# Performance work log

Measured on AMD Instinct MI355X. Metric: run time of the kernel, lower is better.

The kernel has to match this reference:

```python
import jax, jax.numpy as jnp
from jax import lax
import numpy as np

KPAD = 2  # padding for 5x5 kernel, 'same' output

def setup_inputs() -> dict:
    key = jax.random.key(0)
    x = jax.random.normal(key, (16, 8, 512, 512), dtype=jnp.float32)
    # fixed 5x5 averaging kernel, matching torch.ones(5,5)/25
    weight = jnp.ones((1, 1, 5, 5), dtype=jnp.float32) / 25.0
    return {"x": x, "weight": weight}

def reference(x, weight):
    # Per-channel (depthwise) 5x5 box blur. The torch code loops conv2d over
    # split channels; a single grouped conv with feature_group_count=C is the
    # same math in one fused op.
    C = x.shape[1]
    k = jnp.tile(weight, (C, 1, 1, 1))  # (C,1,5,5) OIHW with groups=C
    return lax.conv_general_dilated(
        x, k,
        window_strides=(1, 1),
        padding=[(KPAD, KPAD), (KPAD, KPAD)],
        dimension_numbers=("NCHW", "OIHW", "NCHW"),
        feature_group_count=C,
    )
```

## Files before the change

### kernel.cpp

```cpp
#include <hip/hip_runtime.h>


#define H 512
#define W 512
#define TH 16
#define LROWS (TH + 4)
#define LSTRIDE (W + 8)

__global__ __launch_bounds__(256) void avefilter_kernel(
    const float* __restrict__ x, const float* __restrict__ wgt,
    float* __restrict__ out) {
    __shared__ float smem[LROWS * LSTRIDE];

    const int tid   = threadIdx.x;
    const int r0    = blockIdx.x * TH;
    const int plane = blockIdx.y;

    const float* in   = x   + (size_t)plane * (H * W);
    float*       outp = out + (size_t)plane * (H * W);
    const float scale = wgt[0];

    for (int i = tid; i < LROWS * 8; i += 256) {
        int lr = i >> 3;
        int c  = i & 7;
        int lc = (c < 4) ? c : (W + c);
        smem[lr * LSTRIDE + lc] = 0.0f;
    }

    for (int i = tid; i < LROWS * (W / 4); i += 256) {
        int lr = i >> 7;
        int vc = i & 127;
        int gr = r0 - 2 + lr;
        float4 v = make_float4(0.f, 0.f, 0.f, 0.f);
        if (gr >= 0 && gr < H) {
            v = ((const float4*)(in + (size_t)gr * W))[vc];
        }
        ((float4*)(smem + lr * LSTRIDE + 4))[vc] = v;
    }
    __syncthreads();

    #pragma unroll
    for (int ci = 0; ci < 2; ++ci) {
        const int xcol = tid + ci * 256;
        const float* bcol = smem + xcol + 2;

        float h[5];
        #pragma unroll
        for (int i = 0; i < 5; ++i) {
            const float* b = bcol + i * LSTRIDE;
            h[i] = b[0] + b[1] + b[2] + b[3] + b[4];
        }

        #pragma unroll
        for (int r = 0; r < TH; ++r) {
            float s = h[0] + h[1] + h[2] + h[3] + h[4];
            outp[(size_t)(r0 + r) * W + xcol] = s * scale;
            if (r < TH - 1) {
                const float* b = bcol + (r + 5) * LSTRIDE;
                h[r % 5] = b[0] + b[1] + b[2] + b[3] + b[4];
            }
        }
    }
}

extern "C" void kernel_launch(void* const* d_in, const int* in_sizes, int n_in,
                              void* d_out, int out_size, void* d_ws, size_t ws_size,
                              hipStream_t stream) {
    const float* x   = (const float*)d_in[0];
    const float* wgt = (const float*)d_in[1];
    float* out = (float*)d_out;

    dim3 grid(H / TH, 16 * 8);
    dim3 block(256);
    avefilter_kernel<<<grid, block, 0, stream>>>(x, wgt, out);
}
```

Before: 240.8 us.

## Replace shared-memory tiling with per-wave register strips and lane shuffles

```diff
diff --git a/kernel.cpp b/kernel.cpp
--- a/kernel.cpp
+++ b/kernel.cpp
@@ -3,63 +3,67 @@
 
 #define H 512
 #define W 512
-#define TH 16
-#define LROWS (TH + 4)
-#define LSTRIDE (W + 8)
+#define RSTRIP 16
 
-__global__ __launch_bounds__(256) void avefilter_kernel(
+__global__ __launch_bounds__(256, 4) void avefilter_kernel(
     const float* __restrict__ x, const float* __restrict__ wgt,
-    float* __restrict__ out) {
-    __shared__ float smem[LROWS * LSTRIDE];
-
-    const int tid   = threadIdx.x;
-    const int r0    = blockIdx.x * TH;
-    const int plane = blockIdx.y;
+    float* __restrict__ out)
+{
+    const int lane  = threadIdx.x & 63;
+    const int wave  = threadIdx.x >> 6;
+    const int strip = blockIdx.x * 4 + wave;
+    const int plane = strip >> 5;
+    const int r0    = (strip & 31) * RSTRIP;
 
     const float* in   = x   + (size_t)plane * (H * W);
     float*       outp = out + (size_t)plane * (H * W);
     const float scale = wgt[0];
 
-    for (int i = tid; i < LROWS * 8; i += 256) {
-        int lr = i >> 3;
-        int c  = i & 7;
-        int lc = (c < 4) ? c : (W + c);
-        smem[lr * LSTRIDE + lc] = 0.0f;
-    }
+    const int c0 = lane * 8;
 
-    for (int i = tid; i < LROWS * (W / 4); i += 256) {
-        int lr = i >> 7;
-        int vc = i & 127;
-        int gr = r0 - 2 + lr;
-        float4 v = make_float4(0.f, 0.f, 0.f, 0.f);
+    float hr[5][8];
+
+    auto make_h = [&](int gr, float h[8]) {
+        float v[8];
         if (gr >= 0 && gr < H) {
-            v = ((const float4*)(in + (size_t)gr * W))[vc];
+            const float4* p = (const float4*)(in + (size_t)gr * W + c0);
+            float4 a = p[0], b = p[1];
+            v[0]=a.x; v[1]=a.y; v[2]=a.z; v[3]=a.w;
+            v[4]=b.x; v[5]=b.y; v[6]=b.z; v[7]=b.w;
+        } else {
+            #pragma unroll
+            for (int j = 0; j < 8; ++j) v[j] = 0.f;
         }
-        ((float4*)(smem + lr * LSTRIDE + 4))[vc] = v;
-    }
-    __syncthreads();
+        float l6 = __shfl_up(v[6], 1);
+        float l7 = __shfl_up(v[7], 1);
+        float rA = __shfl_down(v[0], 1);
+        float rB = __shfl_down(v[1], 1);
+        if (lane == 0)  { l6 = 0.f; l7 = 0.f; }
+        if (lane == 63) { rA = 0.f; rB = 0.f; }
+        float e[12];
+        e[0] = l6; e[1] = l7;
+        #pragma unroll
+        for (int j = 0; j < 8; ++j) e[2 + j] = v[j];
+        e[10] = rA; e[11] = rB;
+        #pragma unroll
+        for (int j = 0; j < 8; ++j)
+            h[j] = e[j] + e[j+1] + e[j+2] + e[j+3] + e[j+4];
+    };
 
     #pragma unroll
-    for (int ci = 0; ci < 2; ++ci) {
-        const int xcol = tid + ci * 256;
-        const float* bcol = smem + xcol + 2;
+    for (int k = 0; k < 4; ++k)
+        make_h(r0 - 2 + k, hr[k]);
 
-        float h[5];
+    #pragma unroll
+    for (int r = 0; r < RSTRIP; ++r) {
+        make_h(r0 + 2 + r, hr[(r + 4) % 5]);
+        float o[8];
         #pragma unroll
-        for (int i = 0; i < 5; ++i) {
-            const float* b = bcol + i * LSTRIDE;
-            h[i] = b[0] + b[1] + b[2] + b[3] + b[4];
-        }
-
-        #pragma unroll
-        for (int r = 0; r < TH; ++r) {
-            float s = h[0] + h[1] + h[2] + h[3] + h[4];
-            outp[(size_t)(r0 + r) * W + xcol] = s * scale;
-            if (r < TH - 1) {
-                const float* b = bcol + (r + 5) * LSTRIDE;
-                h[r % 5] = b[0] + b[1] + b[2] + b[3] + b[4];
-            }
-        }
+        for (int j = 0; j < 8; ++j)
+            o[j] = (hr[0][j] + hr[1][j] + hr[2][j] + hr[3][j] + hr[4][j]) * scale;
+        float4* q = (float4*)(outp + (size_t)(r0 + r) * W + c0);
+        q[0] = make_float4(o[0], o[1], o[2], o[3]);
+        q[1] = make_float4(o[4], o[5], o[6], o[7]);
     }
 }
 
@@ -70,7 +74,7 @@
     const float* wgt = (const float*)d_in[1];
     float* out = (float*)d_out;
 
-    dim3 grid(H / TH, 16 * 8);
+    dim3 grid(1024);
     dim3 block(256);
     avefilter_kernel<<<grid, block, 0, stream>>>(x, wgt, out);
 }
```

New measurement: 250.7 us. 1.04x slower.
